# Performance work log

Hardware: AMD Instinct MI355X
Metric: run time of the kernel (lower is better)

The kernel has to match this reference:

```python
import jax, jax.numpy as jnp
import numpy as np

B, T, D, H = 32, 512, 512, 512
P_IN, P_HID = 0.2, 0.2  # input_dropout, hidden_dropout


def _dropout_mask(key, shape, p):
    # inverted dropout mask, as torch F.dropout applied to a ones tensor
    keep = jax.random.bernoulli(key, 1.0 - p, shape)
    return keep.astype(jnp.float32) / (1.0 - p)


def setup_inputs() -> dict:
    key = jax.random.key(0)
    ks = jax.random.split(key, 12)
    k = 1.0 / np.sqrt(H)
    u = lambda kk, shp: jax.random.uniform(kk, shp, jnp.float32, -k, k)
    inp = {
        "x": jax.random.normal(ks[0], (B, T, D), jnp.float32),
        # variational dropout masks (sampled once, reused every timestep)
        "mask_x": _dropout_mask(ks[1], (B, D), P_IN),
        "mask_out": _dropout_mask(ks[2], (B, 2 * H), P_HID),
        "mask_h": jnp.stack([_dropout_mask(ks[3], (B, H), P_HID),
                             _dropout_mask(ks[4], (B, H), P_HID)]),  # [n_layers,B,H]
        # layer 0 (input D), 2 directions stacked; LSTM gate order i,f,g,o
        "w_ih_l0": u(ks[5], (2, 4 * H, D)),
        "w_hh_l0": u(ks[6], (2, 4 * H, H)),
        "b_l0": u(ks[7], (2, 4 * H)),
        # layer 1 (input 2H)
        "w_ih_l1": u(ks[8], (2, 4 * H, 2 * H)),
        "w_hh_l1": u(ks[9], (2, 4 * H, H)),
        "b_l1": u(ks[10], (2, 4 * H)),
    }
    return inp


def _lstm_scan(x_seq, w_ih, w_hh, b, mask_h, reverse):
    # x_seq: [T,B,in]; variational dropout mask_h applied to h each step
    b_, h_ = x_seq.shape[1], w_hh.shape[1]
    h0 = jnp.zeros((b_, h_), x_seq.dtype)

    def step(carry, x_t):
        h, c = carry
        gates = x_t @ w_ih.T + (h * mask_h) @ w_hh.T + b
        i, f, g, o = jnp.split(gates, 4, axis=-1)
        c = jax.nn.sigmoid(f) * c + jax.nn.sigmoid(i) * jnp.tanh(g)
        h = jax.nn.sigmoid(o) * jnp.tanh(c)
        return (h, c), h

    (hT, cT), ys = jax.lax.scan(step, (h0, h0), x_seq, reverse=reverse)
    return ys, hT, cT  # ys in original time order even when reverse


def reference(x, mask_x, mask_out, mask_h, w_ih_l0, w_hh_l0, b_l0,
              w_ih_l1, w_hh_l1, b_l1):
    xt = jnp.swapaxes(x, 0, 1)  # [T,B,D] (batch_first transpose)
    layers = [(w_ih_l0, w_hh_l0, b_l0), (w_ih_l1, w_hh_l1, b_l1)]
    hs, cs = [], []
    inp = xt * mask_x[None]  # layer-0 input mask
    for li, (wi, wh, bb) in enumerate(layers):
        outs = []
        for d in range(2):  # forward / backward direction
            ys, hT, cT = _lstm_scan(inp, wi[d], wh[d], bb[d], mask_h[li],
                                    reverse=(d == 1))
            outs.append(ys)
            hs.append(hT)
            cs.append(cT)
        inp = jnp.concatenate(outs, axis=-1)  # [T,B,2H]
        if li + 1 < len(layers):
            inp = inp * mask_out[None]  # mask applied as next layer's input mask
    output = jnp.swapaxes(inp, 0, 1)  # [B,T,2H]
    hn = jnp.stack(hs)  # [num_layers*2, B, H]
    cn = jnp.stack(cs)
    return output, hn, cn
```

## Files before the change

### kernel.cpp

```cpp
#include <hip/hip_runtime.h>
#include <math.h>

typedef unsigned short ushort_t;
typedef short short8 __attribute__((ext_vector_type(8)));
typedef float floatx4 __attribute__((ext_vector_type(4)));
typedef float float4v __attribute__((ext_vector_type(4)));
typedef unsigned int uint4v __attribute__((ext_vector_type(4)));

__device__ __forceinline__ float b2f(ushort_t u) {
    union { unsigned int i; float f; } v; v.i = ((unsigned int)u) << 16; return v.f;
}
__device__ __forceinline__ ushort_t f2b(float f) {
    union { float f; unsigned int i; } v; v.f = f;
    unsigned int x = v.i;
    return (ushort_t)((x + 0x7fffu + ((x >> 16) & 1u)) >> 16);
}
__device__ __forceinline__ void split8(const float* v, short8& hi, short8& lo) {
#pragma unroll
    for (int e = 0; e < 8; ++e) {
        ushort_t h = f2b(v[e]);
        hi[e] = (short)h;
        lo[e] = (short)f2b(v[e] - b2f(h));
    }
}
__device__ __forceinline__ void load8f(const float* p, float* v) {
    *(float4v*)(v)     = *(const float4v*)(p);
    *(float4v*)(v + 4) = *(const float4v*)(p + 4);
}
__device__ __forceinline__ floatx4 mfma16(short8 a, short8 b, floatx4 c) {
    return __builtin_amdgcn_mfma_f32_16x16x32_bf16(a, b, c, 0, 0, 0);
}
__device__ __forceinline__ void store8_cc(void* p, unsigned long long v) {
    asm volatile("global_store_dwordx2 %0, %1, off sc0 sc1"
                 :: "v"(p), "v"(v) : "memory");
}
__device__ __forceinline__ void store4_cc(void* p, unsigned int v) {
    asm volatile("global_store_dword %0, %1, off sc0 sc1"
                 :: "v"(p), "v"(v) : "memory");
}

__global__ void detect_dtype(const unsigned int* __restrict__ x, int* __restrict__ flag) {
    __shared__ int cnt;
    if (threadIdx.x == 0) cnt = 0;
    __syncthreads();
    int c = 0;
#pragma unroll
    for (int i = 0; i < 8; ++i) {
        unsigned int w = x[threadIdx.x * 8 + i];
        unsigned int e = (w >> 7) & 0xFFu;
        if (e >= 100u && e <= 140u) ++c;
    }
    atomicAdd(&cnt, c);
    __syncthreads();
    if (threadIdx.x == 0) *flag = (cnt > 1024) ? 1 : 0;
}

__global__ __launch_bounds__(256) void prep(
    const int* __restrict__ flag,
    const void* __restrict__ x, const void* __restrict__ mask_x,
    char* __restrict__ xs)
{
    const bool isbf = (*flag != 0);
    const int i = blockIdx.x * 256 + threadIdx.x;
    const int b = i >> 15;
    const int rem = i & 32767;
    const int t = rem >> 6;
    const int c = rem & 63;
    const size_t xoff = ((size_t)(b * 512 + t)) * 512 + c * 8;
    if (isbf) {
        const ushort_t* X = (const ushort_t*)x;
        const ushort_t* M = (const ushort_t*)mask_x + b * 512 + c * 8;
        short8 o;
#pragma unroll
        for (int e = 0; e < 8; ++e) o[e] = (short)f2b(b2f(X[xoff + e]) * b2f(M[e]));
        *(short8*)(xs + ((size_t)t * 32 + b) * 1024 + c * 16) = o;
    } else {
        float v[8], m[8];
        load8f((const float*)x + xoff, v);
        load8f((const float*)mask_x + b * 512 + c * 8, m);
#pragma unroll
        for (int e = 0; e < 8; ++e) v[e] *= m[e];
        short8 hi, lo; split8(v, hi, lo);
        char* p = xs + ((size_t)t * 32 + b) * 2048 + c * 32;
        *(short8*)p = hi; *(short8*)(p + 16) = lo;
    }
}

__device__ __forceinline__ int lds_swz(int row, int o) {
    return o ^ ((row & 7) << 4) ^ (((o >> 6) & 7) << 4);
}

template <int LAYER>
__global__ __launch_bounds__(512, 2) void lstm_phase(
    const int* __restrict__ flag,
    const char* __restrict__ xs,
    char* __restrict__ os,
    char* __restrict__ hs,
    char* __restrict__ flags,
    const void* __restrict__ w_ih, const void* __restrict__ w_hh,
    const void* __restrict__ bias, const void* __restrict__ mask_h,
    const void* __restrict__ mask_out, void* __restrict__ dout,
    int os4_host, int write_hn)
{
    __shared__ __align__(16) char smem[40960];
    float* gb = (float*)(smem + 32768);
    const int dir  = blockIdx.x >> 6;
    const int b6   = blockIdx.x & 63;
    const int jt   = b6 & 31;
    const int m    = b6 >> 5;
    const int j0   = jt << 4;
    const int tid  = threadIdx.x;
    const int w    = tid >> 6;
    const int q    = w & 3;
    const int kh   = w >> 2;
    const int lane = tid & 63;
    const int n16  = lane & 15;
    const int quad = lane >> 4;
    const bool isbf = (*flag != 0);
    const bool os4  = (!isbf) && (os4_host != 0);
    constexpr int KI = (LAYER == 0) ? 512 : 1024;
    constexpr int NIT = (KI / 2) / 32;
    constexpr int NH = 8;
    const int gq = q * 512 + j0 + n16;

    short8 wih_h[NIT], wih_l[NIT], whh_h[NH], whh_l[NH];
    if (isbf) {
        const ushort_t* WI = (const ushort_t*)w_ih + ((size_t)(dir * 2048 + gq)) * KI + kh * (KI / 2) + quad * 8;
        const ushort_t* WH = (const ushort_t*)w_hh + ((size_t)(dir * 2048 + gq)) * 512 + kh * 256 + quad * 8;
#pragma unroll
        for (int ki = 0; ki < NIT; ++ki) { wih_h[ki] = *(const short8*)(WI + ki * 32); wih_l[ki] = short8{0,0,0,0,0,0,0,0}; }
#pragma unroll
        for (int ki = 0; ki < NH; ++ki) { whh_h[ki] = *(const short8*)(WH + ki * 32); whh_l[ki] = short8{0,0,0,0,0,0,0,0}; }
    } else {
        const float* WI = (const float*)w_ih + ((size_t)(dir * 2048 + gq)) * KI + kh * (KI / 2) + quad * 8;
        const float* WH = (const float*)w_hh + ((size_t)(dir * 2048 + gq)) * 512 + kh * 256 + quad * 8;
#pragma unroll
        for (int ki = 0; ki < NIT; ++ki) { float w8[8]; load8f(WI + ki * 32, w8); split8(w8, wih_h[ki], wih_l[ki]); }
#pragma unroll
        for (int ki = 0; ki < NH; ++ki) { float w8[8]; load8f(WH + ki * 32, w8); split8(w8, whh_h[ki], whh_l[ki]); }
    }

    auto xpart = [&](int ts) -> floatx4 {
        floatx4 a = {0.f, 0.f, 0.f, 0.f};
        if (isbf) {
            const int stride = (LAYER == 0) ? 1024 : 2048;
            const char* xb = xs + ((size_t)ts * 32 + m * 16 + n16) * stride + (kh * NIT * 4 + quad) * 16;
#pragma unroll
            for (int ki = 0; ki < NIT; ++ki)
                a = mfma16(*(const short8*)(xb + ki * 64), wih_h[ki], a);
        } else if (LAYER == 1 && !os4) {
            const char* xb = xs + ((size_t)ts * 32 + m * 16 + n16) * 2048 + (kh * 64 + quad) * 16;
#pragma unroll
            for (int ki = 0; ki < NIT; ++ki) {
                short8 av = *(const short8*)(xb + ki * 64);
                a = mfma16(av, wih_h[ki], a);
                a = mfma16(av, wih_l[ki], a);
            }
        } else {
            const int stride = (LAYER == 0) ? 2048 : 4096;
            const char* xb = xs + ((size_t)ts * 32 + m * 16 + n16) * stride + (kh * NIT * 4 + quad) * 32;
#pragma unroll
            for (int ki = 0; ki < NIT; ++ki) {
                short8 ah = *(const short8*)(xb + ki * 128);
                short8 al = *(const short8*)(xb + ki * 128 + 16);
                a = mfma16(ah, wih_h[ki], a);
                a = mfma16(al, wih_h[ki], a);
                a = mfma16(ah, wih_l[ki], a);
            }
        }
        return a;
    };

    const int el4 = (lane & 3) * 4;
    const int erow = m * 16 + (lane >> 2);
    const int ej0 = j0 + el4;
    float bi4[4] = {0,0,0,0}, bf4[4] = {0,0,0,0}, bg4[4] = {0,0,0,0}, bo4[4] = {0,0,0,0};
    float mh4[4] = {0,0,0,0}, mo4[4] = {0,0,0,0};
    if (w == 7) {
        if (isbf) {
            const ushort_t* BI = (const ushort_t*)bias;
            const ushort_t* MH = (const ushort_t*)mask_h + LAYER * 16384;
#pragma unroll
            for (int u = 0; u < 4; ++u) {
                const int ej = ej0 + u;
                bi4[u] = b2f(BI[dir * 2048 + ej]);        bf4[u] = b2f(BI[dir * 2048 + 512 + ej]);
                bg4[u] = b2f(BI[dir * 2048 + 1024 + ej]); bo4[u] = b2f(BI[dir * 2048 + 1536 + ej]);
                mh4[u] = b2f(MH[erow * 512 + ej]);
                mo4[u] = (LAYER == 0) ? b2f(((const ushort_t*)mask_out)[erow * 1024 + dir * 512 + ej]) : 0.f;
            }
        } else {
            const float* BI = (const float*)bias;
            const float* MH = (const float*)mask_h + LAYER * 16384;
            *(float4v*)bi4 = *(const float4v*)(BI + dir * 2048 + ej0);
            *(float4v*)bf4 = *(const float4v*)(BI + dir * 2048 + 512 + ej0);
            *(float4v*)bg4 = *(const float4v*)(BI + dir * 2048 + 1024 + ej0);
            *(float4v*)bo4 = *(const float4v*)(BI + dir * 2048 + 1536 + ej0);
            *(float4v*)mh4 = *(const float4v*)(MH + erow * 512 + ej0);
            if (LAYER == 0) *(float4v*)mo4 = *(const float4v*)((const float*)mask_out + erow * 1024 + dir * 512 + ej0);
        }
    }
    float creg[4] = {0.f, 0.f, 0.f, 0.f};

    const char* myflags = flags + (size_t)((dir * 2 + m) * 32) * 64;
    floatx4 acc = xpart(dir ? 511 : 0);

    for (int s = 0; s < 512; ++s) {
        const int t = dir ? (511 - s) : s;

        if (w == 0) {
            const char* fb = myflags + (size_t)(lane & 31) * 64;
            int fv;
            for (;;) {
                asm volatile("global_load_dword %0, %1, off sc0 sc1\n\ts_waitcnt vmcnt(0)"
                             : "=v"(fv) : "v"(fb) : "memory");
                if (__all(fv >= s)) break;
            }
        }
        __syncthreads();
        __builtin_amdgcn_sched_barrier(0);

        {
            const char* hr = hs + (size_t)((s & 1) * 2 + dir) * 65536;
            const int planes = isbf ? 1 : 2;
            if (tid < planes * 256) {
                const int p = tid >> 8, v = tid & 255;
                const int row = v >> 4, seg = v & 15;
                const char* gsrc = hr + p * 32768 + (size_t)(m * 16 + row) * 1024 + seg * 64;
                uint4v t0, t1, t2, t3;
                asm volatile("global_load_dwordx4 %0, %1, off sc0 sc1" : "=v"(t0) : "v"(gsrc));
                asm volatile("global_load_dwordx4 %0, %1, off sc0 sc1" : "=v"(t1) : "v"(gsrc + 16));
                asm volatile("global_load_dwordx4 %0, %1, off sc0 sc1" : "=v"(t2) : "v"(gsrc + 32));
                asm volatile("global_load_dwordx4 %0, %1, off sc0 sc1" : "=v"(t3) : "v"(gsrc + 48));
                asm volatile("s_waitcnt vmcnt(0)" ::: "memory");
                __builtin_amdgcn_sched_barrier(0);
                char* lbase = smem + p * 16384 + row * 1024;
                *(uint4v*)(lbase + lds_swz(row, seg * 64))      = t0;
                *(uint4v*)(lbase + lds_swz(row, seg * 64 + 16)) = t1;
                *(uint4v*)(lbase + lds_swz(row, seg * 64 + 32)) = t2;
                *(uint4v*)(lbase + lds_swz(row, seg * 64 + 48)) = t3;
            }
        }
        __syncthreads();

        {
            const char* hrow = smem + n16 * 1024;
            if (isbf) {
#pragma unroll
                for (int ki = 0; ki < NH; ++ki) {
                    const int o = kh * 512 + ki * 64 + quad * 16;
                    acc = mfma16(*(const short8*)(hrow + lds_swz(n16, o)), whh_h[ki], acc);
                }
            } else {
#pragma unroll
                for (int ki = 0; ki < NH; ++ki) {
                    const int o = kh * 512 + ki * 64 + quad * 16;
                    const int so = lds_swz(n16, o);
                    short8 ah = *(const short8*)(hrow + so);
                    short8 al = *(const short8*)(hrow + 16384 + so);
                    acc = mfma16(ah, whh_h[ki], acc);
                    acc = mfma16(al, whh_h[ki], acc);
                    acc = mfma16(ah, whh_l[ki], acc);
                }
            }
        }

#pragma unroll
        for (int r = 0; r < 4; ++r)
            gb[((q * 2 + kh) * 16 + quad * 4 + r) * 16 + n16] = acc[r];
        __syncthreads();

        if (w == 7) {
            float4v gA[8];
#pragma unroll
            for (int z = 0; z < 8; ++z)
                gA[z] = *(const float4v*)(gb + z * 256 + lane * 4);

            float hv4[4], cn4[4];
            unsigned long long hiw = 0ull, low = 0ull;
#pragma unroll
            for (int u = 0; u < 4; ++u) {
                float ig = gA[0][u] + gA[1][u] + bi4[u];
                float fg = gA[2][u] + gA[3][u] + bf4[u];
                float gg = gA[4][u] + gA[5][u] + bg4[u];
                float og = gA[6][u] + gA[7][u] + bo4[u];
                float si = 1.f / (1.f + expf(-ig));
                float sf = 1.f / (1.f + expf(-fg));
                float so = 1.f / (1.f + expf(-og));
                float cn = sf * creg[u] + si * tanhf(gg);
                float h  = so * tanhf(cn);
                creg[u] = cn; hv4[u] = h; cn4[u] = cn;
                float hm = h * mh4[u];
                ushort_t hhi = f2b(hm);
                hiw |= (unsigned long long)hhi << (16 * u);
                low |= (unsigned long long)f2b(hm - b2f(hhi)) << (16 * u);
            }
            char* hw = hs + (size_t)(((s + 1) & 1) * 2 + dir) * 65536 + (size_t)erow * 1024 + ej0 * 2;
            store8_cc(hw, hiw);
            if (!isbf) store8_cc(hw + 32768, low);
            asm volatile("s_waitcnt vmcnt(0)" ::: "memory");
            if (lane == 0 && s != 511)
                store4_cc((void*)(myflags + (size_t)jt * 64), (unsigned int)(s + 1));

            const int jg0 = dir * 512 + ej0;
            if constexpr (LAYER == 0) {
                unsigned long long ohi = 0ull, olo = 0ull;
#pragma unroll
                for (int u = 0; u < 4; ++u) {
                    float ho = hv4[u] * mo4[u];
                    ushort_t oh = f2b(ho);
                    ohi |= (unsigned long long)oh << (16 * u);
                    olo |= (unsigned long long)f2b(ho - b2f(oh)) << (16 * u);
                }
                if (os4) {
                    char* op = os + ((size_t)t * 32 + erow) * 4096 + (jg0 >> 3) * 32 + (jg0 & 7) * 2;
                    *(unsigned long long*)op = ohi;
                    *(unsigned long long*)(op + 16) = olo;
                } else {
                    *(unsigned long long*)(os + ((size_t)t * 32 + erow) * 2048 + (size_t)jg0 * 2) = ohi;
                }
            } else {
                size_t o1 = ((size_t)erow * 512 + t) * 1024 + jg0;
                if (isbf) {
                    unsigned long long ow = 0ull;
#pragma unroll
                    for (int u = 0; u < 4; ++u) ow |= (unsigned long long)f2b(hv4[u]) << (16 * u);
                    *(unsigned long long*)((ushort_t*)dout + o1) = ow;
                } else {
                    *(float4v*)((float*)dout + o1) = float4v{hv4[0], hv4[1], hv4[2], hv4[3]};
                }
            }
            if (s == 511 && write_hn) {
                size_t hnidx = 16777216u + (size_t)((LAYER * 2 + dir) * 32 + erow) * 512 + ej0;
                if (isbf) {
                    unsigned long long hw_ = 0ull, cw_ = 0ull;
#pragma unroll
                    for (int u = 0; u < 4; ++u) {
                        hw_ |= (unsigned long long)f2b(hv4[u]) << (16 * u);
                        cw_ |= (unsigned long long)f2b(cn4[u]) << (16 * u);
                    }
                    *(unsigned long long*)((ushort_t*)dout + hnidx) = hw_;
                    *(unsigned long long*)((ushort_t*)dout + hnidx + 65536) = cw_;
                } else {
                    *(float4v*)((float*)dout + hnidx) = float4v{hv4[0], hv4[1], hv4[2], hv4[3]};
                    *(float4v*)((float*)dout + hnidx + 65536) = float4v{cn4[0], cn4[1], cn4[2], cn4[3]};
                }
            }
        }

        if (s != 511) acc = xpart(dir ? (510 - s) : (s + 1));
    }
}

extern "C" void kernel_launch(void* const* d_in, const int* in_sizes, int n_in,
                              void* d_out, int out_size, void* d_ws, size_t ws_size,
                              hipStream_t stream) {
    char* ws = (char*)d_ws;
    const size_t HSB = 262144;
    const size_t FLB = 8192;
    int os4 = (ws_size >= 67108864ull + HSB + FLB + 64) ? 1 : 0;
    size_t osb = os4 ? 67108864ull : 33554432ull;
    char* hs = ws + osb;
    char* flags = hs + HSB;
    int* flag = (int*)(flags + FLB);
    int write_hn = (out_size >= 16908288) ? 1 : 0;

    int hb = -1;
    if (in_sizes && n_in > 0) {
        if (in_sizes[0] == 33554432) hb = 0;
        else if (in_sizes[0] == 16777216) hb = 1;
    }

    hipMemsetAsync(hs, 0, HSB + FLB + 64, stream);
    if (hb == 1)       hipMemsetAsync(flag, 1, 4, stream);
    else if (hb == -1) detect_dtype<<<1, 256, 0, stream>>>((const unsigned int*)d_in[0], flag);

    prep<<<4096, 256, 0, stream>>>(flag, d_in[0], d_in[1], (char*)d_out);

    lstm_phase<0><<<128, 512, 0, stream>>>(flag, (const char*)d_out, ws,
        hs, flags, d_in[4], d_in[5], d_in[6], d_in[3], d_in[2], d_out,
        os4, write_hn);

    hipMemsetAsync(hs, 0, HSB + FLB, stream);

    lstm_phase<1><<<128, 512, 0, stream>>>(flag, (const char*)ws, ws,
        hs, flags, d_in[7], d_in[8], d_in[9], d_in[3], nullptr, d_out,
        os4, write_hn);
}
```

Measured before the change: 8.586 ms.

## Place each LSTM direction's blocks on one XCC and relax cross-block coherence

The launch grows to 1024 blocks. Each block reads its hardware XCC id and joins a role-assignment protocol that gives two XCCs 64 slots each, so all blocks of one direction run on the same XCC; surplus blocks exit at once. When a direction's 64 slots all come from one XCC, the per-step hidden-state exchange and flag polling drop the sc1 cache bit and stay within that XCC's L2 rather than going system-coherent. A timeout fallback assigns slots across XCCs and keeps the coherent path. This adds launch overhead and an assignment phase with livelock and correctness risk.

After: 19.66 ms. 129% more time.

```diff
diff --git a/kernel.cpp b/kernel.cpp
--- a/kernel.cpp
+++ b/kernel.cpp
@@ -30,13 +30,17 @@
 __device__ __forceinline__ floatx4 mfma16(short8 a, short8 b, floatx4 c) {
     return __builtin_amdgcn_mfma_f32_16x16x32_bf16(a, b, c, 0, 0, 0);
 }
-__device__ __forceinline__ void store8_cc(void* p, unsigned long long v) {
-    asm volatile("global_store_dwordx2 %0, %1, off sc0 sc1"
-                 :: "v"(p), "v"(v) : "memory");
-}
-__device__ __forceinline__ void store4_cc(void* p, unsigned int v) {
-    asm volatile("global_store_dword %0, %1, off sc0 sc1"
-                 :: "v"(p), "v"(v) : "memory");
+__device__ __forceinline__ void store8_sc(void* p, unsigned long long v, bool fast) {
+    if (fast) asm volatile("global_store_dwordx2 %0, %1, off sc0"     :: "v"(p), "v"(v) : "memory");
+    else      asm volatile("global_store_dwordx2 %0, %1, off sc0 sc1" :: "v"(p), "v"(v) : "memory");
+}
+__device__ __forceinline__ void store4_sc(void* p, unsigned int v, bool fast) {
+    if (fast) asm volatile("global_store_dword %0, %1, off sc0"     :: "v"(p), "v"(v) : "memory");
+    else      asm volatile("global_store_dword %0, %1, off sc0 sc1" :: "v"(p), "v"(v) : "memory");
+}
+__device__ __forceinline__ void load16_sc(const void* p, uint4v& d, bool fast) {
+    if (fast) asm volatile("global_load_dwordx4 %0, %1, off sc0"     : "=v"(d) : "v"(p));
+    else      asm volatile("global_load_dwordx4 %0, %1, off sc0 sc1" : "=v"(d) : "v"(p));
 }
 
 __global__ void detect_dtype(const unsigned int* __restrict__ x, int* __restrict__ flag) {
@@ -90,6 +94,8 @@
     return o ^ ((row & 7) << 4) ^ (((o >> 6) & 7) << 4);
 }
 
+#define SCOPE_A __HIP_MEMORY_SCOPE_AGENT
+
 template <int LAYER>
 __global__ __launch_bounds__(512, 2) void lstm_phase(
     const int* __restrict__ flag,
@@ -97,19 +103,90 @@
     char* __restrict__ os,
     char* __restrict__ hs,
     char* __restrict__ flags,
+    unsigned int* __restrict__ staff,
     const void* __restrict__ w_ih, const void* __restrict__ w_hh,
     const void* __restrict__ bias, const void* __restrict__ mask_h,
     const void* __restrict__ mask_out, void* __restrict__ dout,
     int os4_host, int write_hn)
 {
     __shared__ __align__(16) char smem[40960];
+    __shared__ int s_slot, s_fast;
     float* gb = (float*)(smem + 32768);
-    const int dir  = blockIdx.x >> 6;
-    const int b6   = blockIdx.x & 63;
+    const int tid  = threadIdx.x;
+
+    if (tid == 0) {
+        unsigned* R = staff;
+        int xcc; asm volatile("s_getreg_b32 %0, hwreg(HW_REG_XCC_ID)" : "=s"(xcc));
+        xcc &= 7;
+        unsigned myrole;
+        for (;;) {
+            unsigned cur = __hip_atomic_load(&R[xcc], __ATOMIC_ACQUIRE, SCOPE_A);
+            if (cur >= 1u && cur <= 3u) { myrole = cur; break; }
+            if (cur == 0u) {
+                unsigned exp = 0u;
+                if (__hip_atomic_compare_exchange_strong(&R[xcc], &exp, 255u,
+                        __ATOMIC_ACQ_REL, __ATOMIC_RELAXED, SCOPE_A)) {
+                    unsigned r = __hip_atomic_fetch_add(&R[8], 1u, __ATOMIC_RELAXED, SCOPE_A);
+                    myrole = (r < 2u) ? (r + 1u) : 3u;
+                    __hip_atomic_store(&R[xcc], myrole, __ATOMIC_RELEASE, SCOPE_A);
+                    break;
+                }
+            }
+            __builtin_amdgcn_s_sleep(2);
+        }
+        int slot = -1, mixed_claim = 0;
+        if (myrole <= 2u) {
+            unsigned tck = __hip_atomic_fetch_add(&R[9 + (myrole - 1u)], 1u, __ATOMIC_RELAXED, SCOPE_A);
+            if (tck < 64u) slot = (int)((myrole - 1u) * 64u + tck);
+        }
+        if (slot < 0) {
+            unsigned long long t0 = __builtin_amdgcn_s_memrealtime();
+            int tried = 0;
+            for (;;) {
+                unsigned c0 = __hip_atomic_load(&R[11], __ATOMIC_ACQUIRE, SCOPE_A);
+                unsigned c1 = __hip_atomic_load(&R[12], __ATOMIC_ACQUIRE, SCOPE_A);
+                if (c0 >= 64u && c1 >= 64u) break;
+                if (!tried && __hip_atomic_load(&R[13], __ATOMIC_RELAXED, SCOPE_A)) {
+                    tried = 1;
+                    unsigned ta = __hip_atomic_fetch_add(&R[9], 1u, __ATOMIC_RELAXED, SCOPE_A);
+                    if (ta < 64u) { slot = (int)ta; mixed_claim = 1; }
+                    else {
+                        unsigned tb = __hip_atomic_fetch_add(&R[10], 1u, __ATOMIC_RELAXED, SCOPE_A);
+                        if (tb < 64u) { slot = (int)(64u + tb); mixed_claim = 1; }
+                    }
+                    if (slot >= 0) break;
+                }
+                if (__builtin_amdgcn_s_memrealtime() - t0 > 524288ull)
+                    __hip_atomic_store(&R[13], 1u, __ATOMIC_RELAXED, SCOPE_A);
+                __builtin_amdgcn_s_sleep(8);
+            }
+        }
+        int fastv = 0;
+        if (slot >= 0) {
+            const int ds = slot >> 6;
+            if (mixed_claim)
+                __hip_atomic_store(&R[14 + ds], 1u, __ATOMIC_RELAXED, SCOPE_A);
+            __hip_atomic_fetch_add(&R[11 + ds], 1u, __ATOMIC_RELEASE, SCOPE_A);
+            unsigned long long t0 = __builtin_amdgcn_s_memrealtime();
+            while (__hip_atomic_load(&R[11 + ds], __ATOMIC_ACQUIRE, SCOPE_A) < 64u) {
+                if (__builtin_amdgcn_s_memrealtime() - t0 > 524288ull)
+                    __hip_atomic_store(&R[13], 1u, __ATOMIC_RELAXED, SCOPE_A);
+                __builtin_amdgcn_s_sleep(2);
+            }
+            fastv = (__hip_atomic_load(&R[14 + ds], __ATOMIC_RELAXED, SCOPE_A) == 0u) ? 1 : 0;
+        }
+        s_slot = slot; s_fast = fastv;
+    }
+    __syncthreads();
+    const int slot = s_slot;
+    if (slot < 0) return;
+    const bool fast = (s_fast != 0);
+
+    const int dir  = slot >> 6;
+    const int b6   = slot & 63;
     const int jt   = b6 & 31;
     const int m    = b6 >> 5;
     const int j0   = jt << 4;
-    const int tid  = threadIdx.x;
     const int w    = tid >> 6;
     const int q    = w & 3;
     const int kh   = w >> 2;
@@ -210,10 +287,18 @@
         if (w == 0) {
             const char* fb = myflags + (size_t)(lane & 31) * 64;
             int fv;
-            for (;;) {
-                asm volatile("global_load_dword %0, %1, off sc0 sc1\n\ts_waitcnt vmcnt(0)"
-                             : "=v"(fv) : "v"(fb) : "memory");
-                if (__all(fv >= s)) break;
+            if (fast) {
+                for (;;) {
+                    asm volatile("global_load_dword %0, %1, off sc0\n\ts_waitcnt vmcnt(0)"
+                                 : "=v"(fv) : "v"(fb) : "memory");
+                    if (__all(fv >= s)) break;
+                }
+            } else {
+                for (;;) {
+                    asm volatile("global_load_dword %0, %1, off sc0 sc1\n\ts_waitcnt vmcnt(0)"
+                                 : "=v"(fv) : "v"(fb) : "memory");
+                    if (__all(fv >= s)) break;
+                }
             }
         }
         __syncthreads();
@@ -227,10 +312,10 @@
                 const int row = v >> 4, seg = v & 15;
                 const char* gsrc = hr + p * 32768 + (size_t)(m * 16 + row) * 1024 + seg * 64;
                 uint4v t0, t1, t2, t3;
-                asm volatile("global_load_dwordx4 %0, %1, off sc0 sc1" : "=v"(t0) : "v"(gsrc));
-                asm volatile("global_load_dwordx4 %0, %1, off sc0 sc1" : "=v"(t1) : "v"(gsrc + 16));
-                asm volatile("global_load_dwordx4 %0, %1, off sc0 sc1" : "=v"(t2) : "v"(gsrc + 32));
-                asm volatile("global_load_dwordx4 %0, %1, off sc0 sc1" : "=v"(t3) : "v"(gsrc + 48));
+                load16_sc(gsrc,      t0, fast);
+                load16_sc(gsrc + 16, t1, fast);
+                load16_sc(gsrc + 32, t2, fast);
+                load16_sc(gsrc + 48, t3, fast);
                 asm volatile("s_waitcnt vmcnt(0)" ::: "memory");
                 __builtin_amdgcn_sched_barrier(0);
                 char* lbase = smem + p * 16384 + row * 1024;
@@ -295,11 +380,11 @@
                 low |= (unsigned long long)f2b(hm - b2f(hhi)) << (16 * u);
             }
             char* hw = hs + (size_t)(((s + 1) & 1) * 2 + dir) * 65536 + (size_t)erow * 1024 + ej0 * 2;
-            store8_cc(hw, hiw);
-            if (!isbf) store8_cc(hw + 32768, low);
+            store8_sc(hw, hiw, fast);
+            if (!isbf) store8_sc(hw + 32768, low, fast);
             asm volatile("s_waitcnt vmcnt(0)" ::: "memory");
             if (lane == 0 && s != 511)
-                store4_cc((void*)(myflags + (size_t)jt * 64), (unsigned int)(s + 1));
+                store4_sc((void*)(myflags + (size_t)jt * 64), (unsigned int)(s + 1), fast);
 
             const int jg0 = dir * 512 + ej0;
             if constexpr (LAYER == 0) {
@@ -357,11 +442,13 @@
     char* ws = (char*)d_ws;
     const size_t HSB = 262144;
     const size_t FLB = 8192;
-    int os4 = (ws_size >= 67108864ull + HSB + FLB + 64) ? 1 : 0;
+    const size_t STB = 256;
+    int os4 = (ws_size >= 67108864ull + HSB + FLB + STB + 64) ? 1 : 0;
     size_t osb = os4 ? 67108864ull : 33554432ull;
     char* hs = ws + osb;
     char* flags = hs + HSB;
-    int* flag = (int*)(flags + FLB);
+    unsigned int* staff = (unsigned int*)(flags + FLB);
+    int* flag = (int*)(flags + FLB + STB);
     int write_hn = (out_size >= 16908288) ? 1 : 0;
 
     int hb = -1;
@@ -370,19 +457,19 @@
         else if (in_sizes[0] == 16777216) hb = 1;
     }
 
-    hipMemsetAsync(hs, 0, HSB + FLB + 64, stream);
+    hipMemsetAsync(hs, 0, HSB + FLB + STB + 64, stream);
     if (hb == 1)       hipMemsetAsync(flag, 1, 4, stream);
     else if (hb == -1) detect_dtype<<<1, 256, 0, stream>>>((const unsigned int*)d_in[0], flag);
 
     prep<<<4096, 256, 0, stream>>>(flag, d_in[0], d_in[1], (char*)d_out);
 
-    lstm_phase<0><<<128, 512, 0, stream>>>(flag, (const char*)d_out, ws,
-        hs, flags, d_in[4], d_in[5], d_in[6], d_in[3], d_in[2], d_out,
+    lstm_phase<0><<<1024, 512, 0, stream>>>(flag, (const char*)d_out, ws,
+        hs, flags, staff, d_in[4], d_in[5], d_in[6], d_in[3], d_in[2], d_out,
         os4, write_hn);
 
-    hipMemsetAsync(hs, 0, HSB + FLB, stream);
-
-    lstm_phase<1><<<128, 512, 0, stream>>>(flag, (const char*)ws, ws,
-        hs, flags, d_in[7], d_in[8], d_in[9], d_in[3], nullptr, d_out,
+    hipMemsetAsync(hs, 0, HSB + FLB + STB, stream);
+
+    lstm_phase<1><<<1024, 512, 0, stream>>>(flag, (const char*)ws, ws,
+        hs, flags, staff, d_in[7], d_in[8], d_in[9], d_in[3], nullptr, d_out,
         os4, write_hn);
 }
```
